# Kernel tuning notes

Measured on AMD Instinct MI355X. Metric: run time of the kernel, lower is better.

Reference implementation:

```python
import jax, jax.numpy as jnp
import numpy as np

D_MODEL = 1024
D_INNER = 2048      # expand * d_model
D_STATE = 64
HEADDIM = 128
NHEADS = 16         # d_inner // headdim
D_CONV = 4
CHUNK = 256
D_IN_PROJ = 2 * D_INNER + 2 * D_STATE + NHEADS   # 4240 (ngroups=1)
CONV_DIM = D_INNER + 2 * D_STATE                 # 2176
EPS = 1e-5


def setup_inputs() -> dict:
    key = jax.random.key(0)
    ks = jax.random.split(key, 8)
    B, L = 2, 4096
    u = jax.random.normal(ks[0], (B, L, D_MODEL), jnp.float32)
    in_proj_w = jax.random.normal(ks[1], (D_IN_PROJ, D_MODEL), jnp.float32) / np.sqrt(D_MODEL)
    conv_w = jax.random.uniform(ks[2], (CONV_DIM, D_CONV), jnp.float32, -0.5, 0.5)
    conv_b = jnp.zeros((CONV_DIM,), jnp.float32)
    # dt_bias init exactly as in the module: inv-softplus of dt ~ logU(1e-3, 1e-1)
    dt0 = jnp.exp(jax.random.uniform(ks[3], (NHEADS,), jnp.float32) * (np.log(0.1) - np.log(0.001)) + np.log(0.001))
    dt_bias = dt0 + jnp.log(-jnp.expm1(-dt0))
    A_log = jnp.log(jax.random.uniform(ks[4], (NHEADS,), jnp.float32, 1.0, 16.0))
    Dp = jnp.ones((NHEADS,), jnp.float32)
    norm_w = jnp.ones((D_INNER,), jnp.float32)
    out_proj_w = jax.random.normal(ks[5], (D_MODEL, D_INNER), jnp.float32) / np.sqrt(D_INNER)
    return dict(u=u, in_proj_w=in_proj_w, conv_w=conv_w, conv_b=conv_b, dt_bias=dt_bias,
                A_log=A_log, Dp=Dp, norm_w=norm_w, out_proj_w=out_proj_w)


def _ssd(x, dt, A, Bm, Cm, Dp):
    # Chunked selective state-space scan (mamba_chunk_scan_combined semantics).
    # x: [b,l,h,p], dt: [b,l,h] (already softplus'd), A: [h] (negative), Bm/Cm: [b,l,n]
    b, l, h, p = x.shape
    n = Bm.shape[-1]
    nc = l // CHUNK
    xc = x.reshape(b, nc, CHUNK, h, p)
    dtc = dt.reshape(b, nc, CHUNK, h)
    Bc = Bm.reshape(b, nc, CHUNK, n)
    Cc = Cm.reshape(b, nc, CHUNK, n)
    a = dtc * A                       # [b,c,q,h], a <= 0
    acum = jnp.cumsum(a, axis=2)      # within-chunk cumulative log-decay
    # ---- intra-chunk (causal, attention-like) ----
    scores = jnp.einsum('bcqn,bckn->bcqk', Cc, Bc)
    diff = acum[:, :, :, None, :] - acum[:, :, None, :, :]        # [b,c,q,k,h]
    mask = jnp.tril(jnp.ones((CHUNK, CHUNK), bool))[None, None, :, :, None]
    decay = jnp.exp(jnp.where(mask, diff, -jnp.inf))
    M = scores[..., None] * decay * dtc[:, :, None, :, :]         # [b,c,q,k,h]
    y_diag = jnp.einsum('bcqkh,bckhp->bcqhp', M, xc)
    # ---- per-chunk end states ----
    decay_states = jnp.exp(acum[:, :, -1:, :] - acum)             # [b,c,q,h]
    states = jnp.einsum('bcqh,bcqn,bcqhp->bchpn', dtc * decay_states, Bc, xc)
    # ---- inter-chunk recurrence (scan over nc chunks) ----
    chunk_decay = jnp.exp(acum[:, :, -1, :])                      # [b,c,h]
    def step(s, inp):
        st, cd = inp
        return cd[:, :, None, None] * s + st, s                   # emit state BEFORE this chunk
    init = jnp.zeros((b, h, p, n), x.dtype)
    _, prev = jax.lax.scan(step, init, (states.transpose(1, 0, 2, 3, 4), chunk_decay.transpose(1, 0, 2)))
    prev = prev.transpose(1, 0, 2, 3, 4)                          # [b,c,h,p,n]
    y_off = jnp.einsum('bcqn,bchpn,bcqh->bcqhp', Cc, prev, jnp.exp(acum))
    y = y_diag + y_off + xc * Dp[None, None, None, :, None]
    return y.reshape(b, l, h, p)


def _forward(u, in_proj_w, conv_w, conv_b, dt_bias, A_log, Dp, norm_w, out_proj_w):
    b, l, _ = u.shape
    zxbct = jnp.einsum('bld,ed->ble', u, in_proj_w)
    z = zxbct[..., :D_INNER]
    xBC = zxbct[..., D_INNER:D_INNER + CONV_DIM]
    dt = zxbct[..., D_INNER + CONV_DIM:]
    dt = jax.nn.softplus(dt + dt_bias)                            # [b,l,h]
    # causal depthwise conv1d (padding d_conv-1, truncated to seq_len) + SiLU
    xp = jnp.pad(xBC, ((0, 0), (D_CONV - 1, 0), (0, 0)))
    conv_out = conv_b
    for w in range(D_CONV):
        conv_out = conv_out + xp[:, w:w + l, :] * conv_w[:, w]
    xBC = jax.nn.silu(conv_out)
    x = xBC[..., :D_INNER]
    Bm = xBC[..., D_INNER:D_INNER + D_STATE]
    Cm = xBC[..., D_INNER + D_STATE:]
    A = -jnp.exp(A_log)
    y = _ssd(x.reshape(b, l, NHEADS, HEADDIM), dt, A, Bm, Cm, Dp)
    y = y.reshape(b, l, D_INNER)
    # RMSNormGated (norm_before_gate=False): gate first, then RMSNorm
    y = y * jax.nn.silu(z)
    y = y * jax.lax.rsqrt(jnp.mean(y * y, axis=-1, keepdims=True) + EPS) * norm_w
    return jnp.einsum('ble,de->bld', y, out_proj_w)


def reference(u, in_proj_w, conv_w, conv_b, dt_bias, A_log, Dp, norm_w, out_proj_w):
    return _forward(u, in_proj_w, conv_w, conv_b, dt_bias, A_log, Dp, norm_w, out_proj_w)
```

## Files before the change

kernel.cpp:

```cpp
#include <hip/hip_runtime.h>
#include <hip/hip_bf16.h>
#include <cstdint>
#include <cstddef>

#define D_MODEL   1024
#define D_INNER   2048
#define D_STATE   64
#define HEADDIM   128
#define NHEADS    16
#define D_CONV    4
#define CHUNK     256
#define D_IN_PROJ 4240
#define ZPAD      4352
#define CONV_DIM  2176
#define NB        2
#define LEN       4096
#define NC        16
#define MROWS     (NB*LEN)

typedef __hip_bfloat16 bf16;
typedef __bf16 bf16x8 __attribute__((ext_vector_type(8)));
typedef float  f32x4  __attribute__((ext_vector_type(4)));
typedef unsigned short us4 __attribute__((ext_vector_type(4)));

__device__ __forceinline__ float fsilu(float x){ return x / (1.f + __expf(-x)); }
__device__ __forceinline__ float toF(float x){ return x; }
__device__ __forceinline__ float toF(bf16 x){ return __bfloat162float(x); }
__device__ __forceinline__ void storeF(float* p, float v){ *p = v; }
__device__ __forceinline__ void storeF(bf16* p, float v){ *p = __float2bfloat16(v); }

__device__ __forceinline__ unsigned short f2bs(float v){
  return __bfloat16_as_ushort(__float2bfloat16(v));
}
__device__ __forceinline__ void store4(bf16* p, f32x4 v){
  us4 o; o[0]=f2bs(v[0]); o[1]=f2bs(v[1]); o[2]=f2bs(v[2]); o[3]=f2bs(v[3]);
  *(us4*)p = o;
}
__device__ __forceinline__ void store4(float* p, f32x4 v){
  *(f32x4*)p = v;
}

__device__ __forceinline__ void gload_lds16(const void* g, void* l){
  __builtin_amdgcn_global_load_lds(
     (const __attribute__((address_space(1))) unsigned int*)(uintptr_t)g,
     (__attribute__((address_space(3))) unsigned int*)(uintptr_t)l, 16, 0, 0);
}

template<typename TC>
__global__ __launch_bounds__(256, 2) void k_gemm_pipe(
    const bf16* __restrict__ A, int lda,
    const bf16* __restrict__ B, int ldb,
    TC* __restrict__ C, int ldc, int K)
{
  __shared__ __align__(16) char lds[3*24576];
  const int tid  = threadIdx.x;
  const int w    = tid >> 6, l = tid & 63;
  const int quad = l >> 4, lq = l & 15;
  const int wm   = (w >> 1)*128, wn = (w & 1)*64;

  const int m0 = blockIdx.x*256, n0 = blockIdx.y*128;

  const int rs = tid >> 2;
  const int cs = ((tid & 3) ^ (rs & 3)) * 8;
  const bf16* Ag = A + (size_t)(m0 + rs)*lda + cs;
  const bf16* Bg = B + (size_t)(n0 + rs)*ldb + cs;
  const int sdo = w*1024;

  auto stage = [&](int k0, char* bufb){
    #pragma unroll
    for (int p=0;p<4;p++)
      gload_lds16(Ag + (size_t)p*64*lda + k0, bufb + p*4096 + sdo);
    #pragma unroll
    for (int p=0;p<2;p++)
      gload_lds16(Bg + (size_t)p*64*ldb + k0, bufb + 16384 + p*4096 + sdo);
  };

  char* bufA = lds;
  char* bufB = lds + 24576;
  char* bufC = lds + 49152;

  f32x4 acc[8][4] = {};
  const int sl  = (quad ^ (lq & 3)) * 16;
  const int aro = (wm + lq)*64;
  const int bro = 16384 + (wn + lq)*64;

  stage(0,  bufA);
  stage(32, bufB);
  asm volatile("s_waitcnt vmcnt(6)" ::: "memory");
  __builtin_amdgcn_s_barrier();
  asm volatile("" ::: "memory");

  const int NT = K >> 5;
  for (int t = 0; t < NT; ++t){
    if (t + 2 < NT) stage((t+2) << 5, bufC);

    bf16x8 af[8], bfr[4];
    #pragma unroll
    for (int m=0;m<8;m++) af[m]  = *(const bf16x8*)(bufA + aro + m*1024 + sl);
    #pragma unroll
    for (int n=0;n<4;n++) bfr[n] = *(const bf16x8*)(bufA + bro + n*1024 + sl);

    __builtin_amdgcn_s_setprio(1);
    #pragma unroll
    for (int m=0;m<8;m++)
      #pragma unroll
      for (int n=0;n<4;n++)
        acc[m][n] = __builtin_amdgcn_mfma_f32_16x16x32_bf16(bfr[n], af[m], acc[m][n], 0,0,0);
    __builtin_amdgcn_s_setprio(0);

    if (t < NT-1){
      __builtin_amdgcn_sched_barrier(0);
      if (t == NT-2) { asm volatile("s_waitcnt vmcnt(0)" ::: "memory"); }
      else           { asm volatile("s_waitcnt vmcnt(6)" ::: "memory"); }
      __builtin_amdgcn_s_barrier();
      asm volatile("" ::: "memory");
    }
    char* tmp = bufA; bufA = bufB; bufB = bufC; bufC = tmp;
  }

  #pragma unroll
  for (int m=0;m<8;m++){
    const int r = m0 + wm + m*16 + lq;
    #pragma unroll
    for (int n=0;n<4;n++){
      const int cb = n0 + wn + n*16 + quad*4;
      store4(&C[(size_t)r*ldc + cb], acc[m][n]);
    }
  }
}

#define NU4  (MROWS*D_MODEL/4)
#define NW14 (ZPAD*D_MODEL/4)
#define NW24 (D_MODEL*D_INNER/4)
__global__ __launch_bounds__(256) void k_convert(
    const float* __restrict__ u, const float* __restrict__ Win,
    const float* __restrict__ Wout, const float* __restrict__ norm_w,
    bf16* __restrict__ ub, bf16* __restrict__ Wb_in, bf16* __restrict__ Wb_out){
  int i4 = blockIdx.x*256 + threadIdx.x;
  if (i4 < NU4){
    float4 v = ((const float4*)u)[i4];
    us4 o = {f2bs(v.x), f2bs(v.y), f2bs(v.z), f2bs(v.w)};
    ((us4*)ub)[i4] = o;
  } else if (i4 < NU4 + NW14){
    int j = i4 - NU4;
    int r = j >> 8;
    float4 v = make_float4(0.f,0.f,0.f,0.f);
    if (r < D_IN_PROJ) v = ((const float4*)Win)[j];
    us4 o = {f2bs(v.x), f2bs(v.y), f2bs(v.z), f2bs(v.w)};
    ((us4*)Wb_in)[j] = o;
  } else {
    int j = i4 - NU4 - NW14;
    float4 v = ((const float4*)Wout)[j];
    float4 nw = ((const float4*)norm_w)[j & 511];
    us4 o = {f2bs(v.x*nw.x), f2bs(v.y*nw.y), f2bs(v.z*nw.z), f2bs(v.w*nw.w)};
    ((us4*)Wb_out)[j] = o;
  }
}

__global__ __launch_bounds__(256) void k_dt(
    const bf16* __restrict__ zxbct, const float* __restrict__ dt_bias,
    const float* __restrict__ A_log, float* __restrict__ dt_t,
    float* __restrict__ acum_t, float* __restrict__ cd_t){
  int bid = blockIdx.x;
  int h = bid & 15, c = (bid>>4)&15, b = bid>>8;
  int q = threadIdx.x;
  size_t m = (size_t)(b*NC + c)*CHUNK + q;
  float x = toF(zxbct[m*ZPAD + (D_INNER + CONV_DIM) + h]) + dt_bias[h];
  float dtv = (x > 20.f) ? x : log1pf(__expf(x));
  float Ah = -__expf(A_log[h]);
  float a = dtv * Ah;
  __shared__ float sb[CHUNK];
  sb[q] = a;
  __syncthreads();
  #pragma unroll
  for (int off=1; off<CHUNK; off<<=1){
    float t = (q >= off) ? sb[q-off] : 0.f;
    __syncthreads();
    sb[q] += t;
    __syncthreads();
  }
  float ac = sb[q];
  size_t o = ((size_t)(b*NHEADS+h))*LEN + c*CHUNK + q;
  dt_t[o]   = dtv;
  acum_t[o] = ac;
  if (q == CHUNK-1) cd_t[(b*NHEADS+h)*NC + c] = __expf(ac);
}

__global__ __launch_bounds__(256) void k_conv(
    const bf16* __restrict__ zxbct, const float* __restrict__ conv_w,
    const float* __restrict__ conv_b, bf16* __restrict__ xbc){
  __shared__ __align__(16) __bf16 xs[67*64];
  __shared__ __align__(16) float  ws[64*4];
  __shared__ float bs[64];
  const int tid = threadIdx.x;
  const int cq = tid & 7;
  const int tm = tid >> 3;
  const int c0 = blockIdx.x*64;
  const int m0 = blockIdx.y*64;
  {
    int g = m0 - 3 + tm; if (g < 0) g = 0;
    *(bf16x8*)&xs[tm*64 + cq*8] =
        *(const bf16x8*)(zxbct + (size_t)g*ZPAD + D_INNER + c0 + cq*8);
    int g2 = m0 - 3 + tm + 32;
    *(bf16x8*)&xs[(tm+32)*64 + cq*8] =
        *(const bf16x8*)(zxbct + (size_t)g2*ZPAD + D_INNER + c0 + cq*8);
    if (tid < 24){
      int r3 = 64 + (tid >> 3);
      int g3 = m0 - 3 + r3;
      *(bf16x8*)&xs[r3*64 + cq*8] =
          *(const bf16x8*)(zxbct + (size_t)g3*ZPAD + D_INNER + c0 + cq*8);
    }
  }
  if (tid < 64)      *(float4*)&ws[tid*4] = *(const float4*)(conv_w + (size_t)(c0+tid)*4);
  else if (tid < 128) bs[tid-64] = conv_b[c0 + tid - 64];
  __syncthreads();

  #pragma unroll
  for (int rr=0; rr<2; rr++){
    const int r = tm + rr*32;
    const int m = m0 + r;
    const int l = m & (LEN-1);
    float acc[8];
    #pragma unroll
    for (int j=0;j<8;j++) acc[j] = bs[cq*8+j];
    #pragma unroll
    for (int w=0; w<D_CONV; w++){
      if (l - (D_CONV-1) + w >= 0){
        bf16x8 v = *(const bf16x8*)&xs[(r+w)*64 + cq*8];
        #pragma unroll
        for (int j=0;j<8;j++) acc[j] += (float)v[j] * ws[(cq*8+j)*4 + w];
      }
    }
    bf16x8 o;
    #pragma unroll
    for (int j=0;j<8;j++) o[j] = (__bf16)fsilu(acc[j]);
    *(bf16x8*)(xbc + (size_t)m*CONV_DIM + c0 + cq*8) = o;
  }
}

__global__ __launch_bounds__(256,2) void k_states(
    const bf16* __restrict__ xbc, const float* __restrict__ acum_t,
    const float* __restrict__ dt_t, float* __restrict__ states)
{
  const int bid = blockIdx.x;
  const int h = bid & 15, c = (bid>>4)&15, b = bid>>8;
  const int z = b*NC + c;
  const int tid = threadIdx.x;
  const int w = tid >> 6, l = tid & 63;
  const int quad = l >> 4, lq = l & 15;

  __shared__ __align__(16) __bf16 xsT[2][128*72];
  __shared__ __align__(16) __bf16 bts[2][64*72];

  const float* acum = acum_t + ((size_t)(b*NHEADS+h))*LEN + c*CHUNK;
  const float* dtc  = dt_t   + ((size_t)(b*NHEADS+h))*LEN + c*CHUNK;
  const float alast = acum[CHUNK-1];
  const bf16* xrow = xbc + (size_t)z*CHUNK*CONV_DIM + h*HEADDIM;
  const bf16* Brow = xbc + (size_t)z*CHUNK*CONV_DIM + D_INNER;

  f32x4 Sst[2][4] = {};

  auto stage = [&](int t, int buf){
    const int k0 = t*64;
    const bf16* xr = xrow + (size_t)(k0+l)*CONV_DIM;
    #pragma unroll
    for (int pass=0; pass<4; pass++){
      int pb = w*8 + pass*32;
      bf16x8 v = *(const bf16x8*)(xr + pb);
      #pragma unroll
      for (int j=0;j<8;j++) xsT[buf][(pb+j)*72 + l] = v[j];
    }
    float wl = dtc[k0+l] * __expf(alast - acum[k0+l]);
    const bf16* br = Brow + (size_t)(k0+l)*CONV_DIM;
    #pragma unroll
    for (int pass=0; pass<2; pass++){
      int nb = w*8 + pass*32;
      bf16x8 v = *(const bf16x8*)(br + nb);
      #pragma unroll
      for (int j=0;j<8;j++) bts[buf][(nb+j)*72 + l] = (__bf16)((float)v[j] * wl);
    }
  };

  stage(0, 0);
  for (int t = 0; t < 4; t++){
    const int buf = t & 1;
    __syncthreads();
    if (t < 3) stage(t+1, buf^1);
    #pragma unroll
    for (int s=0;s<2;s++){
      bf16x8 a2[2];
      #pragma unroll
      for (int mi=0;mi<2;mi++)
        a2[mi] = *(const bf16x8*)&xsT[buf][(w*32 + mi*16 + lq)*72 + s*32 + quad*8];
      #pragma unroll
      for (int ni=0;ni<4;ni++){
        bf16x8 bb = *(const bf16x8*)&bts[buf][(ni*16+lq)*72 + s*32 + quad*8];
        #pragma unroll
        for (int mi=0;mi<2;mi++)
          Sst[mi][ni] = __builtin_amdgcn_mfma_f32_16x16x32_bf16(bb, a2[mi], Sst[mi][ni], 0,0,0);
      }
    }
  }

  float* so = states + (size_t)bid*HEADDIM*D_STATE;
  #pragma unroll
  for (int mi=0;mi<2;mi++){
    int pp = w*32 + mi*16 + lq;
    #pragma unroll
    for (int ni=0;ni<4;ni++)
      store4(&so[pp*D_STATE + ni*16 + quad*4], Sst[mi][ni]);
  }
}

__global__ __launch_bounds__(256) void k_scan(
    const float* __restrict__ states, const float* __restrict__ cd_t,
    bf16* __restrict__ prevb){
  int b = blockIdx.x >> 4, h = blockIdx.x & 15;
  int pt = blockIdx.y;
  int tid = threadIdx.x;
  float carry[4] = {0.f,0.f,0.f,0.f};
  for (int c=0;c<NC;c++){
    size_t base = ((size_t)(b*256 + c*16 + h))*HEADDIM*D_STATE + (size_t)pt*1024;
    float cd = cd_t[(b*NHEADS+h)*NC + c];
    #pragma unroll
    for (int i=0;i<4;i++){
      size_t idx = base + (size_t)i*256 + tid;
      prevb[idx] = __float2bfloat16(carry[i]);
      carry[i] = carry[i]*cd + states[idx];
    }
  }
}

__global__ __launch_bounds__(256,2) void k_fused(
    const bf16* __restrict__ xbc, const float* __restrict__ acum_t,
    const float* __restrict__ dt_t, const float* __restrict__ Dp,
    const bf16* __restrict__ prevb, bf16* __restrict__ y)
{
  const int bid = blockIdx.x;
  const int h = bid & 15, c = (bid>>4)&15, b = bid>>8;
  const int z = b*NC + c;
  const int tid = threadIdx.x;
  const int w = tid >> 6, l = tid & 63;
  const int quad = l >> 4, lq = l & 15;

  __shared__ __align__(16) __bf16 xsT[2][128*72];
  __shared__ __align__(16) __bf16 Ms[4][32*40];
  __shared__ float acs[CHUNK], dts[CHUNK];

  const float* acum = acum_t + ((size_t)(b*NHEADS+h))*LEN + c*CHUNK;
  const float* dtc  = dt_t   + ((size_t)(b*NHEADS+h))*LEN + c*CHUNK;
  acs[tid] = acum[tid];
  dts[tid] = dtc[tid];

  const bf16* xrow = xbc + (size_t)z*CHUNK*CONV_DIM + h*HEADDIM;
  const bf16* Brow = xbc + (size_t)z*CHUNK*CONV_DIM + D_INNER;
  const bf16* Crow = xbc + (size_t)z*CHUNK*CONV_DIM + D_INNER + D_STATE;
  const bf16* pv   = prevb + (size_t)bid*HEADDIM*D_STATE;
  const float Dph = Dp[h];
  const int j0 = w, j1 = 7 - w;

  f32x4 Yacc[2][2][8] = {};

  auto stage = [&](int t, int buf){
    const bf16* xr = xrow + (size_t)(t*64+l)*CONV_DIM;
    #pragma unroll
    for (int pass=0; pass<4; pass++){
      int pb = w*8 + pass*32;
      bf16x8 v = *(const bf16x8*)(xr + pb);
      #pragma unroll
      for (int j=0;j<8;j++) xsT[buf][(pb+j)*72 + l] = v[j];
    }
  };

  stage(0, 0);
  __syncthreads();

  #pragma unroll
  for (int s=0;s<2;s++){
    bf16x8 bp[8];
    #pragma unroll
    for (int pn=0;pn<8;pn++)
      bp[pn] = *(const bf16x8*)(pv + (pn*16+lq)*D_STATE + s*32 + quad*8);
    #pragma unroll
    for (int half=0; half<2; half++){
      const int j = half ? j1 : j0;
      #pragma unroll
      for (int qm=0;qm<2;qm++){
        int row = j*32 + qm*16 + lq;
        float e = __expf(acs[row]);
        bf16x8 a = *(const bf16x8*)(Crow + (size_t)row*CONV_DIM + s*32 + quad*8);
        bf16x8 ae;
        #pragma unroll
        for (int jj=0;jj<8;jj++) ae[jj] = (__bf16)((float)a[jj] * e);
        #pragma unroll
        for (int pn=0;pn<8;pn++)
          Yacc[half][qm][pn] = __builtin_amdgcn_mfma_f32_16x16x32_bf16(bp[pn], ae, Yacc[half][qm][pn], 0,0,0);
      }
    }
  }

  for (int t = 0; t < 4; t++){
    const int buf = t & 1;
    if (t > 0) __syncthreads();
    if (t < 3) stage(t+1, buf^1);

    #pragma unroll
    for (int half=0; half<2; half++){
      const int j = half ? j1 : j0;
      if (2*t > j) continue;
      const int qbase = j*32;
      bf16x8 cf[2][2];
      #pragma unroll
      for (int s=0;s<2;s++)
        #pragma unroll
        for (int qm=0;qm<2;qm++)
          cf[s][qm] = *(const bf16x8*)(Crow + (size_t)(qbase+qm*16+lq)*CONV_DIM + s*32 + quad*8);
      #pragma unroll
      for (int kk=0; kk<2; kk++){
        const int kh = 2*t + kk;
        if (kh > j) continue;
        const int kb32  = kk*32;
        const int kbase = kh*32;
        f32x4 Sacc[2][2] = {};
        #pragma unroll
        for (int s=0;s<2;s++){
          bf16x8 bfk[2];
          #pragma unroll
          for (int kn=0;kn<2;kn++)
            bfk[kn] = *(const bf16x8*)(Brow + (size_t)(kbase+kn*16+lq)*CONV_DIM + s*32 + quad*8);
          #pragma unroll
          for (int kn=0;kn<2;kn++)
            #pragma unroll
            for (int qm=0;qm<2;qm++)
              Sacc[kn][qm] = __builtin_amdgcn_mfma_f32_16x16x32_bf16(bfk[kn], cf[s][qm], Sacc[kn][qm], 0,0,0);
        }
        #pragma unroll
        for (int qm=0;qm<2;qm++){
          int ql = qbase + qm*16 + lq;
          float aq = acs[ql];
          #pragma unroll
          for (int kn=0;kn<2;kn++){
            us4 o;
            #pragma unroll
            for (int i=0;i<4;i++){
              int kl = kbase + kn*16 + quad*4 + i;
              float v = Sacc[kn][qm][i] * __expf(aq - acs[kl]) * dts[kl];
              v = (kl < ql) ? v : ((kl == ql) ? v + Dph : 0.f);
              o[i] = f2bs(v);
            }
            *(us4*)&Ms[w][(qm*16+lq)*40 + kn*16 + quad*4] = o;
          }
        }
        asm volatile("s_waitcnt lgkmcnt(0)" ::: "memory");
        #pragma unroll
        for (int qm=0;qm<2;qm++){
          bf16x8 am = *(const bf16x8*)&Ms[w][(qm*16+lq)*40 + quad*8];
          #pragma unroll
          for (int pn=0;pn<8;pn++){
            bf16x8 bp = *(const bf16x8*)&xsT[buf][(pn*16+lq)*72 + kb32 + quad*8];
            Yacc[half][qm][pn] = __builtin_amdgcn_mfma_f32_16x16x32_bf16(bp, am, Yacc[half][qm][pn], 0,0,0);
          }
        }
      }
    }
  }

  bf16* yrow = y + (size_t)z*CHUNK*D_INNER + h*HEADDIM;
  #pragma unroll
  for (int half=0; half<2; half++){
    const int j = half ? j1 : j0;
    #pragma unroll
    for (int qm=0;qm<2;qm++){
      int q = j*32 + qm*16 + lq;
      #pragma unroll
      for (int pn=0;pn<8;pn++)
        store4(&yrow[(size_t)q*D_INNER + pn*16 + quad*4], Yacc[half][qm][pn]);
    }
  }
}

__global__ __launch_bounds__(256) void k_gatenorm(
    const bf16* __restrict__ zxbct, bf16* __restrict__ y){
  int m = blockIdx.x;
  int e0 = threadIdx.x*8;
  bf16x8 zv = *(const bf16x8*)(zxbct + (size_t)m*ZPAD + e0);
  bf16x8 yv = *(const bf16x8*)(y + (size_t)m*D_INNER + e0);
  float v[8]; float ss = 0.f;
  #pragma unroll
  for (int j=0;j<8;j++){
    float val = (float)yv[j] * fsilu((float)zv[j]);
    v[j] = val; ss += val*val;
  }
  #pragma unroll
  for (int off=32; off>0; off>>=1) ss += __shfl_down(ss, off, 64);
  __shared__ float red[4];
  if ((threadIdx.x & 63) == 0) red[threadIdx.x >> 6] = ss;
  __syncthreads();
  float tot = red[0]+red[1]+red[2]+red[3];
  float r = rsqrtf(tot * (1.f/D_INNER) + 1e-5f);
  bf16x8 o;
  #pragma unroll
  for (int j=0;j<8;j++) o[j] = (__bf16)(v[j] * r);
  *(bf16x8*)(y + (size_t)m*D_INNER + e0) = o;
}

extern "C" void kernel_launch(void* const* d_in, const int* in_sizes, int n_in,
                              void* d_out, int out_size, void* d_ws, size_t ws_size,
                              hipStream_t stream) {
  const float* u         = (const float*)d_in[0];
  const float* in_proj_w = (const float*)d_in[1];
  const float* conv_w    = (const float*)d_in[2];
  const float* conv_b    = (const float*)d_in[3];
  const float* dt_bias   = (const float*)d_in[4];
  const float* A_log     = (const float*)d_in[5];
  const float* Dp        = (const float*)d_in[6];
  const float* norm_w    = (const float*)d_in[7];
  const float* out_proj_w= (const float*)d_in[8];
  float* out = (float*)d_out;

  char* p = (char*)d_ws;
  auto alloc = [&](size_t bytes){ char* r = p; p += (bytes + 255) & ~size_t(255); return r; };
  bf16*  zxbct = (bf16*) alloc((size_t)MROWS*ZPAD*2);
  bf16*  xbc   = (bf16*) alloc((size_t)MROWS*CONV_DIM*2);
  bf16*  y     = (bf16*) alloc((size_t)MROWS*D_INNER*2);
  bf16*  ub    = (bf16*) alloc((size_t)MROWS*D_MODEL*2);
  bf16*  Wb_in = (bf16*) alloc((size_t)ZPAD*D_MODEL*2);
  bf16*  Wb_out= (bf16*) alloc((size_t)D_MODEL*D_INNER*2);
  float* dt_t  = (float*)alloc((size_t)NB*NHEADS*LEN*4);
  float* acum_t= (float*)alloc((size_t)NB*NHEADS*LEN*4);
  float* cd_t  = (float*)alloc((size_t)NB*NHEADS*NC*4);
  float* states= (float*)ub;
  bf16*  prevb = (bf16*)Wb_in;

  dim3 blk(256);
  k_convert<<<dim3((NU4+NW14+NW24)/256), blk, 0, stream>>>(
      u, in_proj_w, out_proj_w, norm_w, ub, Wb_in, Wb_out);

  k_gemm_pipe<bf16><<<dim3(32, 34), dim3(256), 0, stream>>>(
      ub, D_MODEL, Wb_in, D_MODEL, zxbct, ZPAD, D_MODEL);

  k_dt    <<<dim3(NB*NC*NHEADS), blk, 0, stream>>>(zxbct, dt_bias, A_log, dt_t, acum_t, cd_t);
  k_conv  <<<dim3(CONV_DIM/64, MROWS/64), blk, 0, stream>>>(zxbct, conv_w, conv_b, xbc);
  k_states<<<dim3(NB*NC*NHEADS), blk, 0, stream>>>(xbc, acum_t, dt_t, states);
  k_scan  <<<dim3(NB*NHEADS, 8), blk, 0, stream>>>(states, cd_t, prevb);
  k_fused <<<dim3(NB*NC*NHEADS), blk, 0, stream>>>(xbc, acum_t, dt_t, Dp, prevb, y);
  k_gatenorm<<<dim3(MROWS), blk, 0, stream>>>(zxbct, y);

  k_gemm_pipe<float><<<dim3(32, 8), dim3(256), 0, stream>>>(
      y, D_INNER, Wb_out, D_INNER, out, D_MODEL, D_INNER);
}
```

Measured before the change: 362.7 us.

## Add 8-wave 256x256-tile GEMM with interleaved loads for input projection

```diff
diff --git a/kernel.cpp b/kernel.cpp
--- a/kernel.cpp
+++ b/kernel.cpp
@@ -26,8 +26,6 @@
 __device__ __forceinline__ float fsilu(float x){ return x / (1.f + __expf(-x)); }
 __device__ __forceinline__ float toF(float x){ return x; }
 __device__ __forceinline__ float toF(bf16 x){ return __bfloat162float(x); }
-__device__ __forceinline__ void storeF(float* p, float v){ *p = v; }
-__device__ __forceinline__ void storeF(bf16* p, float v){ *p = __float2bfloat16(v); }
 
 __device__ __forceinline__ unsigned short f2bs(float v){
   return __bfloat16_as_ushort(__float2bfloat16(v));
@@ -44,6 +42,101 @@
   __builtin_amdgcn_global_load_lds(
      (const __attribute__((address_space(1))) unsigned int*)(uintptr_t)g,
      (__attribute__((address_space(3))) unsigned int*)(uintptr_t)l, 16, 0, 0);
+}
+
+template<typename TC>
+__global__ __launch_bounds__(512, 2) void k_gemm_8p(
+    const bf16* __restrict__ A, int lda,
+    const bf16* __restrict__ B, int ldb,
+    TC* __restrict__ C, int ldc, int K)
+{
+  __shared__ __align__(16) char lds[2][4][16384];
+  const int tid  = threadIdx.x;
+  const int w    = tid >> 6, l = tid & 63;
+  const int quad = l >> 4, lq = l & 15;
+  const int wmo  = (w >> 2)*128, wno = (w & 3)*64;
+  const int m0   = blockIdx.x*256, n0 = blockIdx.y*256;
+
+  const int rs = tid >> 2;
+  const int cs = ((tid & 3) ^ ((rs >> 1) & 3)) * 8;
+  const bf16* Ag = A + (size_t)(m0 + rs)*lda + cs;
+  const bf16* Bg = B + (size_t)(n0 + rs)*ldb + cs;
+  const int sdo = w*1024;
+
+#define STAGE_A(t, kh, d) { const int k0_=(t)*64+(kh)*32; char* hb_=&lds[d][(kh)*2][0]; \
+    gload_lds16(Ag + k0_, hb_ + sdo); gload_lds16(Ag + (size_t)128*lda + k0_, hb_ + 8192 + sdo); }
+#define STAGE_B(t, kh, d) { const int k0_=(t)*64+(kh)*32; char* hb_=&lds[d][(kh)*2+1][0]; \
+    gload_lds16(Bg + k0_, hb_ + sdo); gload_lds16(Bg + (size_t)128*ldb + k0_, hb_ + 8192 + sdo); }
+
+  const int slot = (quad ^ ((lq >> 1) & 3)) * 16;
+  const int arow = (wmo + lq)*64;
+  const int brow = (wno + lq)*64;
+
+  f32x4 acc[8][4] = {};
+
+  STAGE_A(0,0,0); STAGE_B(0,0,0); STAGE_A(0,1,0); STAGE_B(0,1,0);
+  asm volatile("s_waitcnt vmcnt(4)" ::: "memory");
+  asm volatile("s_barrier" ::: "memory");
+
+  const int NT = K >> 6;
+  for (int t = 0; t < NT; ++t){
+    const int d  = t & 1;
+    const bool st = (t+1 < NT);
+    bf16x8 af[8], bfr[4];
+    #pragma unroll
+    for (int ks=0; ks<2; ks++){
+      const char* ah = &lds[d][ks*2][0];
+      const char* bh = &lds[d][ks*2+1][0];
+      #pragma unroll
+      for (int m=0;m<8;m++) af[m]  = *(const bf16x8*)(ah + arow + m*1024 + slot);
+      #pragma unroll
+      for (int n=0;n<2;n++) bfr[n] = *(const bf16x8*)(bh + brow + n*1024 + slot);
+      if (st) STAGE_A(t+1, ks, d^1);
+      asm volatile("s_barrier" ::: "memory");
+      __builtin_amdgcn_s_setprio(1);
+      __builtin_amdgcn_sched_barrier(0);
+      #pragma unroll
+      for (int m=0;m<8;m++)
+        #pragma unroll
+        for (int n=0;n<2;n++)
+          acc[m][n] = __builtin_amdgcn_mfma_f32_16x16x32_bf16(bfr[n], af[m], acc[m][n], 0,0,0);
+      __builtin_amdgcn_sched_barrier(0);
+      __builtin_amdgcn_s_setprio(0);
+      asm volatile("s_barrier" ::: "memory");
+      #pragma unroll
+      for (int n=2;n<4;n++) bfr[n] = *(const bf16x8*)(bh + brow + n*1024 + slot);
+      if (st) STAGE_B(t+1, ks, d^1);
+      asm volatile("s_barrier" ::: "memory");
+      __builtin_amdgcn_s_setprio(1);
+      __builtin_amdgcn_sched_barrier(0);
+      #pragma unroll
+      for (int m=0;m<8;m++)
+        #pragma unroll
+        for (int n=2;n<4;n++)
+          acc[m][n] = __builtin_amdgcn_mfma_f32_16x16x32_bf16(bfr[n], af[m], acc[m][n], 0,0,0);
+      __builtin_amdgcn_sched_barrier(0);
+      __builtin_amdgcn_s_setprio(0);
+      if (ks==0){
+        if (st) { asm volatile("s_waitcnt vmcnt(4)" ::: "memory"); }
+        else    { asm volatile("s_waitcnt vmcnt(0)" ::: "memory"); }
+      } else if (st) {
+        asm volatile("s_waitcnt vmcnt(4)" ::: "memory");
+      }
+      asm volatile("s_barrier" ::: "memory");
+    }
+  }
+#undef STAGE_A
+#undef STAGE_B
+
+  #pragma unroll
+  for (int m=0;m<8;m++){
+    const int r = m0 + wmo + m*16 + lq;
+    #pragma unroll
+    for (int n=0;n<4;n++){
+      const int cb = n0 + wno + n*16 + quad*4;
+      store4(&C[(size_t)r*ldc + cb], acc[m][n]);
+    }
+  }
 }
 
 template<typename TC>
@@ -61,7 +154,7 @@
   const int m0 = blockIdx.x*256, n0 = blockIdx.y*128;
 
   const int rs = tid >> 2;
-  const int cs = ((tid & 3) ^ (rs & 3)) * 8;
+  const int cs = ((tid & 3) ^ ((rs >> 1) & 3)) * 8;
   const bf16* Ag = A + (size_t)(m0 + rs)*lda + cs;
   const bf16* Bg = B + (size_t)(n0 + rs)*ldb + cs;
   const int sdo = w*1024;
@@ -80,15 +173,14 @@
   char* bufC = lds + 49152;
 
   f32x4 acc[8][4] = {};
-  const int sl  = (quad ^ (lq & 3)) * 16;
+  const int sl  = (quad ^ ((lq >> 1) & 3)) * 16;
   const int aro = (wm + lq)*64;
   const int bro = 16384 + (wn + lq)*64;
 
   stage(0,  bufA);
   stage(32, bufB);
   asm volatile("s_waitcnt vmcnt(6)" ::: "memory");
-  __builtin_amdgcn_s_barrier();
-  asm volatile("" ::: "memory");
+  asm volatile("s_barrier" ::: "memory");
 
   const int NT = K >> 5;
   for (int t = 0; t < NT; ++t){
@@ -112,8 +204,7 @@
       __builtin_amdgcn_sched_barrier(0);
       if (t == NT-2) { asm volatile("s_waitcnt vmcnt(0)" ::: "memory"); }
       else           { asm volatile("s_waitcnt vmcnt(6)" ::: "memory"); }
-      __builtin_amdgcn_s_barrier();
-      asm volatile("" ::: "memory");
+      asm volatile("s_barrier" ::: "memory");
     }
     char* tmp = bufA; bufA = bufB; bufB = bufC; bufC = tmp;
   }
@@ -536,7 +627,7 @@
   k_convert<<<dim3((NU4+NW14+NW24)/256), blk, 0, stream>>>(
       u, in_proj_w, out_proj_w, norm_w, ub, Wb_in, Wb_out);
 
-  k_gemm_pipe<bf16><<<dim3(32, 34), dim3(256), 0, stream>>>(
+  k_gemm_8p<bf16><<<dim3(32, 17), dim3(512), 0, stream>>>(
       ub, D_MODEL, Wb_in, D_MODEL, zxbct, ZPAD, D_MODEL);
 
   k_dt    <<<dim3(NB*NC*NHEADS), blk, 0, stream>>>(zxbct, dt_bias, A_log, dt_t, acum_t, cd_t);
```

Result: slower. 374.3 us (+3.2%).
